# Optimization experiments

Measured on AMD Instinct MI355X. Metric: run time of the kernel, lower is better.

## Reference

```python
import jax, jax.numpy as jnp
import numpy as np

NUM_HEADS = 16

def setup_inputs() -> dict:
    key = jax.random.key(0)
    ks = jax.random.split(key, 6)
    B, N, E = 2, 2048, 2048
    QK, V, M = 2048, 2048, 4096
    x = jax.random.normal(ks[0], (B, N, E), dtype=jnp.float32)
    Wq = jax.random.normal(ks[1], (QK, E), dtype=jnp.float32) * 0.02
    k_weight = jax.random.normal(ks[2], (M, QK), dtype=jnp.float32) * 0.05
    v_weight = jax.random.normal(ks[3], (M, V), dtype=jnp.float32) * 0.05
    Wg = jax.random.normal(ks[4], (V, E), dtype=jnp.float32) * 0.02
    Wout = jax.random.normal(ks[5], (E, V), dtype=jnp.float32) * 0.02
    return {"x": x, "Wq": Wq, "k_weight": k_weight, "v_weight": v_weight, "Wg": Wg, "Wout": Wout}

def reference(x, Wq, k_weight, v_weight, Wg, Wout):
    H = NUM_HEADS
    B, N, E = x.shape
    M = k_weight.shape[0]
    # q: [B, N, QK] -> [B, H, N, dk]
    q = jnp.einsum('bne,fe->bnf', x, Wq)
    dk = q.shape[-1] // H
    q = q.reshape(B, N, H, dk).transpose(0, 2, 1, 3)
    # k: [M, QK] -> [H, M, dk]; v: [M, V] -> [H, M, dv]
    k = k_weight.reshape(M, H, dk).transpose(1, 0, 2)
    dv = v_weight.shape[1] // H
    v = v_weight.reshape(M, H, dv).transpose(1, 0, 2)
    scale = jnp.asarray(dk, x.dtype) ** 0.5  # use_scale == 1
    k = k * scale
    v = v * scale
    # non-softmax attention over fixed memory
    energy = jax.nn.silu(jnp.einsum('bhnd,hmd->bhnm', q, k))  # [B,H,N,M]
    out = jnp.einsum('bhnm,hmd->bhnd', energy, v)  # [B,H,N,dv]
    out = out.transpose(0, 2, 1, 3).reshape(B, N, H * dv)
    # output gate (silu)
    gate = jax.nn.silu(jnp.einsum('bne,ve->bnv', x, Wg))
    out = out * gate
    return jnp.einsum('bnv,ev->bne', out, Wout)
```

## Files before the change

kernel.cpp:

```cpp
#include <hip/hip_runtime.h>

typedef __bf16 bf16;
typedef __bf16 bf16x4 __attribute__((ext_vector_type(4)));
typedef __bf16 bf16x8 __attribute__((ext_vector_type(8)));
typedef float f32x4 __attribute__((ext_vector_type(4)));

#define MFMA(a, b, c) __builtin_amdgcn_mfma_f32_16x16x32_bf16(a, b, c, 0, 0, 0)

__device__ __forceinline__ float fast_silu(float x) {
  float e = __builtin_amdgcn_exp2f(x * -1.4426950408889634f);
  return x * __builtin_amdgcn_rcpf(1.f + e);
}

__device__ __forceinline__ void gload_lds16(const void* g, void* l) {
  __builtin_amdgcn_global_load_lds(
      (const __attribute__((address_space(1))) void*)g,
      (__attribute__((address_space(3))) void*)l, 16, 0, 0);
}

__global__ __launch_bounds__(256) void cvt_bf16(const float* __restrict__ in,
                                                bf16* __restrict__ out, int n) {
  int i = (blockIdx.x * 256 + threadIdx.x) * 4;
  if (i >= n) return;
  float4 v = *(const float4*)(in + i);
  bf16x4 o = {(bf16)v.x, (bf16)v.y, (bf16)v.z, (bf16)v.w};
  *(bf16x4*)(out + i) = o;
}

__global__ __launch_bounds__(256) void transpose_v_cvt(const float* __restrict__ v,
                                                       bf16* __restrict__ vt) {
  __shared__ bf16 T[64 * 72];
  const int m0 = blockIdx.x * 64, c0 = blockIdx.y * 64;
  const int tid = threadIdx.x;
  const int tr = tid >> 3;
  const int tc = (tid & 7) << 3;
#pragma unroll
  for (int it = 0; it < 2; it++) {
    int r = tr + it * 32;
    const float* src = v + (long)(m0 + r) * 2048 + c0 + tc;
    float4 a = *(const float4*)src;
    float4 b = *(const float4*)(src + 4);
    bf16x8 t = {(bf16)a.x, (bf16)a.y, (bf16)a.z, (bf16)a.w,
                (bf16)b.x, (bf16)b.y, (bf16)b.z, (bf16)b.w};
    *(bf16x8*)&T[r * 72 + tc] = t;
  }
  __syncthreads();
#pragma unroll
  for (int it = 0; it < 2; it++) {
    int c = tr + it * 32;
    bf16x8 o;
#pragma unroll
    for (int j = 0; j < 8; j++) o[j] = T[(tc + j) * 72 + c];
    *(bf16x8*)(vt + (long)(c0 + c) * 4096 + m0 + tc) = o;
  }
}

template <int MODE, int BM>
__global__ __launch_bounds__(512, 2) void gemm256(const bf16* __restrict__ A,
                                                  const bf16* __restrict__ B,
                                                  const bf16* __restrict__ B2,
                                                  bf16* __restrict__ C1,
                                                  bf16* __restrict__ C2,
                                                  float* __restrict__ Cf, int K, int N) {
  constexpr int MR = BM / 32;
  constexpr int MR2 = MR / 2;
  constexpr int NA = BM / 64;
  __shared__ bf16 As[2][BM * 64];
  __shared__ bf16 Bs[2][256 * 64];

  const int tid = threadIdx.x, wave = tid >> 6, lane = tid & 63;
  const int wr = wave >> 2, wc = wave & 3;
  const int quad = lane >> 4, fr = lane & 15;

  const int id2 = (blockIdx.x & 7) * 32 + (blockIdx.x >> 3);
  const int gx = (MODE == 3) ? (id2 >> 4) : (id2 >> 5);
  const int gy = (MODE == 3) ? (id2 & 15) : (id2 & 31);
  const bool gsel = (MODE == 3) && (gx >= 8);
  const bf16* Bm = gsel ? B2 : B;
  const long bM = (long)gy * BM;
  const long bN = (long)((MODE == 3) ? (gx & 7) : gx) * 256;

  f32x4 acc[MR][4] = {};

  const int srow = tid >> 3;
  const int sblk = (tid & 7) ^ (srow & 7);
  const bf16* Ag = A + (bM + srow) * (long)K + (sblk << 3);
  const bf16* Bg = Bm + (bN + srow) * (long)K + (sblk << 3);
  const int sdst = srow * 64 + ((tid & 7) << 3);

  auto stA = [&](int kt, int sb, int i) {
    gload_lds16(Ag + (long)i * 64 * K + kt * 64, &As[sb][sdst + i * 64 * 64]);
  };
  auto stB = [&](int kt, int sb, int i) {
    gload_lds16(Bg + (long)i * 64 * K + kt * 64, &Bs[sb][sdst + i * 64 * 64]);
  };
  auto rdA = [&](int rb, int mi, int kk) {
    int row = wr * (BM / 2) + mi * 16 + fr;
    return *(const bf16x8*)&As[rb][row * 64 + (((kk * 4 + quad) ^ (fr & 7)) << 3)];
  };
  auto rdB = [&](int rb, int ni, int kk) {
    int row = wc * 64 + ni * 16 + fr;
    return *(const bf16x8*)&Bs[rb][row * 64 + (((kk * 4 + quad) ^ (fr & 7)) << 3)];
  };

#pragma unroll
  for (int i = 0; i < NA; i++) stA(0, 0, i);
#pragma unroll
  for (int i = 0; i < 4; i++) stB(0, 0, i);
  __syncthreads();

  const int NT = K >> 6;
  for (int kt = 0; kt < NT; ++kt) {
    const int rb = kt & 1, sb = rb ^ 1;
    const bool st = (kt + 1) < NT;
    bf16x8 bfv[4][2], ah[MR2][2];

#pragma unroll
    for (int ni = 0; ni < 4; ni++)
#pragma unroll
      for (int kk = 0; kk < 2; kk++) bfv[ni][kk] = rdB(rb, ni, kk);
#pragma unroll
    for (int mi = 0; mi < MR2; mi++)
#pragma unroll
      for (int kk = 0; kk < 2; kk++) ah[mi][kk] = rdA(rb, mi, kk);
    if (st) {
      if (BM == 256) { stA(kt + 1, sb, 0); stA(kt + 1, sb, 1); }
      else { stA(kt + 1, sb, 0); stB(kt + 1, sb, 0); }
    }
    __builtin_amdgcn_s_barrier();
    __builtin_amdgcn_s_setprio(1);
#pragma unroll
    for (int mi = 0; mi < MR2; mi++)
#pragma unroll
      for (int ni = 0; ni < 2; ni++)
#pragma unroll
        for (int kk = 0; kk < 2; kk++) acc[mi][ni] = MFMA(ah[mi][kk], bfv[ni][kk], acc[mi][ni]);
    __builtin_amdgcn_s_setprio(0);
    __builtin_amdgcn_s_barrier();

    if (st) {
      if (BM == 256) { stA(kt + 1, sb, 2); stA(kt + 1, sb, 3); }
      else { stA(kt + 1, sb, 1); stB(kt + 1, sb, 1); }
    }
    __builtin_amdgcn_s_barrier();
    __builtin_amdgcn_s_setprio(1);
#pragma unroll
    for (int mi = 0; mi < MR2; mi++)
#pragma unroll
      for (int ni = 2; ni < 4; ni++)
#pragma unroll
        for (int kk = 0; kk < 2; kk++) acc[mi][ni] = MFMA(ah[mi][kk], bfv[ni][kk], acc[mi][ni]);
    __builtin_amdgcn_s_setprio(0);
    __builtin_amdgcn_s_barrier();

#pragma unroll
    for (int mi = 0; mi < MR2; mi++)
#pragma unroll
      for (int kk = 0; kk < 2; kk++) ah[mi][kk] = rdA(rb, mi + MR2, kk);
    if (st) {
      if (BM == 256) { stB(kt + 1, sb, 0); stB(kt + 1, sb, 1); }
      else { stB(kt + 1, sb, 2); }
    }
    __builtin_amdgcn_s_barrier();
    __builtin_amdgcn_s_setprio(1);
#pragma unroll
    for (int mi = 0; mi < MR2; mi++)
#pragma unroll
      for (int ni = 0; ni < 2; ni++)
#pragma unroll
        for (int kk = 0; kk < 2; kk++)
          acc[mi + MR2][ni] = MFMA(ah[mi][kk], bfv[ni][kk], acc[mi + MR2][ni]);
    __builtin_amdgcn_s_setprio(0);
    __builtin_amdgcn_s_barrier();

    if (st) {
      if (BM == 256) { stB(kt + 1, sb, 2); stB(kt + 1, sb, 3); }
      else { stB(kt + 1, sb, 3); }
    }
    __builtin_amdgcn_s_barrier();
    __builtin_amdgcn_s_setprio(1);
#pragma unroll
    for (int mi = 0; mi < MR2; mi++)
#pragma unroll
      for (int ni = 2; ni < 4; ni++)
#pragma unroll
        for (int kk = 0; kk < 2; kk++)
          acc[mi + MR2][ni] = MFMA(ah[mi][kk], bfv[ni][kk], acc[mi + MR2][ni]);
    __builtin_amdgcn_s_setprio(0);
    __syncthreads();
  }

#pragma unroll
  for (int mi = 0; mi < MR; mi++)
#pragma unroll
    for (int ni = 0; ni < 4; ni++)
#pragma unroll
      for (int r = 0; r < 4; r++) {
        long row = bM + wr * (BM / 2) + mi * 16 + quad * 4 + r;
        long col = bN + wc * 64 + ni * 16 + fr;
        float v = acc[mi][ni][r];
        if (MODE == 2) {
          Cf[row * (long)N + col] = v;
        } else {
          if (gsel)
            C2[row * (long)N + col] = (bf16)fast_silu(v);
          else
            C1[row * (long)N + col] = (bf16)(v * 11.3137085f);
        }
      }
}

__global__ __launch_bounds__(512, 4) void attn_fused(const bf16* __restrict__ q,
                                                     const bf16* __restrict__ kw,
                                                     const bf16* __restrict__ vt,
                                                     bf16* __restrict__ gate_io) {
  constexpr int E = 2048, M = 4096;
  constexpr float scale = 11.3137085f;
  const int bid = blockIdx.x;
  const int h = ((bid & 7) << 1) | ((bid >> 8) & 1);
  const int sub = (bid >> 3) & 31;
  const int b = sub >> 4, nt = sub & 15;
  const long n0 = (long)b * 2048 + nt * 128;

  const int tid = threadIdx.x, wave = tid >> 6, lane = tid & 63;
  const int quad = lane >> 4, ln = lane & 15;
  const int sw_m = wave & 1, sw_n = wave >> 1;
  const int pw_n = wave & 3, pw_dv = wave >> 2;

  __shared__ bf16 Ks[2][64 * 128];
  __shared__ bf16 Vts[2][128 * 64];
  __shared__ bf16 Ps[128 * 64];

  const bf16* qbase = q + (n0 + sw_n * 32) * E + h * 128;
  bf16x8 qf[2][4];
#pragma unroll
  for (int n2 = 0; n2 < 2; n2++)
#pragma unroll
    for (int ks = 0; ks < 4; ks++)
      qf[n2][ks] = *(const bf16x8*)(qbase + (long)(n2 * 16 + ln) * E + ks * 32 + (quad << 3));

  f32x4 oacc[2][4] = {};

  const bf16* kg = kw + (long)((wave << 3) + quad) * E + h * 128;
  const int ksl_off = (wave << 3) * 128 + lane * 8;
  int kc[2];
#pragma unroll
  for (int i = 0; i < 2; i++) kc[i] = (ln ^ ((wave * 8 + i * 4 + quad) & 15)) << 3;

  const bf16* vg = vt + (long)(h * 128 + (wave << 4) + (lane >> 3)) * M +
                   (((lane & 7) ^ ((lane >> 3) & 7)) << 3);
  const int vsl_off = (wave << 4) * 64 + lane * 8;

  int waddr[2][2];
#pragma unroll
  for (int mt = 0; mt < 2; mt++)
#pragma unroll
    for (int n2 = 0; n2 < 2; n2++) {
      int n = sw_n * 32 + n2 * 16 + ln;
      int mb8 = sw_m * 4 + mt * 2 + (quad >> 1);
      waddr[mt][n2] = n * 64 + ((mb8 ^ (n & 7)) << 3) + ((quad & 1) << 2);
    }

  auto stage = [&](int ms, int sb) {
#pragma unroll
    for (int i = 0; i < 2; i++) {
      gload_lds16(kg + (long)(ms + i * 4) * E + kc[i], &Ks[sb][ksl_off + i * 4 * 128]);
      gload_lds16(vg + ms + (long)i * 8 * M, &Vts[sb][vsl_off + i * 8 * 64]);
    }
  };

  stage(0, 0);
  asm volatile("s_waitcnt vmcnt(0)" ::: "memory");
  __builtin_amdgcn_s_barrier();

  auto body = [&](int m0, int rb, int sb, bool doStage) {
    if (doStage) stage(m0 + 64, sb);

    f32x4 sacc[2][2] = {};
    __builtin_amdgcn_s_setprio(1);
#pragma unroll
    for (int ks = 0; ks < 4; ks++) {
      bf16x8 af[2];
#pragma unroll
      for (int mt = 0; mt < 2; mt++)
        af[mt] = *(const bf16x8*)&Ks[rb][(sw_m * 32 + mt * 16 + ln) * 128 +
                                         (((ks * 4 + quad) ^ ln) << 3)];
#pragma unroll
      for (int mt = 0; mt < 2; mt++)
#pragma unroll
        for (int n2 = 0; n2 < 2; n2++) sacc[mt][n2] = MFMA(af[mt], qf[n2][ks], sacc[mt][n2]);
    }
    __builtin_amdgcn_s_setprio(0);

#pragma unroll
    for (int mt = 0; mt < 2; mt++)
#pragma unroll
      for (int n2 = 0; n2 < 2; n2++) {
        bf16x4 p;
#pragma unroll
        for (int r = 0; r < 4; r++) p[r] = (bf16)fast_silu(sacc[mt][n2][r]);
        *(bf16x4*)&Ps[waddr[mt][n2]] = p;
      }

    asm volatile("s_waitcnt lgkmcnt(0)" ::: "memory");
    __builtin_amdgcn_s_barrier();

#pragma unroll
    for (int ks = 0; ks < 2; ks++) {
      const int so = ((ks * 4 + quad) ^ (ln & 7)) << 3;
      bf16x8 pf[2], vf[4];
#pragma unroll
      for (int n2 = 0; n2 < 2; n2++)
        pf[n2] = *(const bf16x8*)&Ps[(pw_n * 32 + n2 * 16 + ln) * 64 + so];
#pragma unroll
      for (int dt = 0; dt < 4; dt++)
        vf[dt] = *(const bf16x8*)&Vts[rb][(pw_dv * 64 + dt * 16 + ln) * 64 + so];
      __builtin_amdgcn_s_setprio(1);
#pragma unroll
      for (int n2 = 0; n2 < 2; n2++)
#pragma unroll
        for (int dt = 0; dt < 4; dt++) oacc[n2][dt] = MFMA(pf[n2], vf[dt], oacc[n2][dt]);
      __builtin_amdgcn_s_setprio(0);
    }

    asm volatile("s_waitcnt vmcnt(0)" ::: "memory");
    __builtin_amdgcn_s_barrier();
  };

  for (int m0 = 0; m0 < M; m0 += 128) {
    body(m0, 0, 1, true);
    body(m0 + 64, 1, 0, m0 + 128 < M);
  }

  bf16* gio = gate_io + n0 * E + h * 128;
#pragma unroll
  for (int n2 = 0; n2 < 2; n2++)
#pragma unroll
    for (int dt = 0; dt < 4; dt++)
#pragma unroll
      for (int r = 0; r < 4; r++) {
        int n = pw_n * 32 + n2 * 16 + quad * 4 + r;
        int dv = pw_dv * 64 + dt * 16 + ln;
        float g = (float)gio[(long)n * E + dv];
        gio[(long)n * E + dv] = (bf16)(g * oacc[n2][dt][r] * scale);
      }
}

extern "C" void kernel_launch(void* const* d_in, const int* in_sizes, int n_in,
                              void* d_out, int out_size, void* d_ws, size_t ws_size,
                              hipStream_t stream) {
  const float* x = (const float*)d_in[0];
  const float* Wq = (const float*)d_in[1];
  const float* kw = (const float*)d_in[2];
  const float* vw = (const float*)d_in[3];
  const float* Wg = (const float*)d_in[4];
  const float* Wout = (const float*)d_in[5];
  float* out = (float*)d_out;
  bf16* ws = (bf16*)d_ws;

  bf16* S0 = ws;
  bf16* S1 = ws + 8388608;
  bf16* S2 = ws + 16777216;
  bf16* S3 = ws + 25165824;
  bf16* S4 = ws + 33554432;
  bf16* Wgb = S1 + 4194304;

  cvt_bf16<<<8192, 256, 0, stream>>>(x, S0, 8388608);
  cvt_bf16<<<4096, 256, 0, stream>>>(Wq, S1, 4194304);
  cvt_bf16<<<4096, 256, 0, stream>>>(Wg, Wgb, 4194304);
  transpose_v_cvt<<<dim3(64, 32), 256, 0, stream>>>(vw, S2);
  gemm256<3, 256><<<256, 512, 0, stream>>>(S0, S1, Wgb, S3, S4, (float*)nullptr, 2048, 2048);
  cvt_bf16<<<8192, 256, 0, stream>>>(kw, S0, 8388608);
  attn_fused<<<512, 512, 0, stream>>>(S3, S0, S2, S4);
  cvt_bf16<<<4096, 256, 0, stream>>>(Wout, S1, 4194304);
  gemm256<2, 128><<<256, 512, 0, stream>>>(S4, S1, (const bf16*)nullptr, (bf16*)nullptr,
                                           (bf16*)nullptr, out, 2048, 2048);
}
```

Before: 460.3 us.

## Triple-buffer A tiles and issue all prefetches at iteration start with vmcnt waits

The GEMM main loop now triple-buffers the A tile and double-buffers B in LDS. All global-to-LDS loads for the next B tile and the A tile two steps ahead are issued at the top of each iteration, instead of being spread across four phases with extra barriers. The full __syncthreads is replaced by a partial s_waitcnt vmcnt plus s_barrier, so the A prefetch for kt+2 stays in flight across iterations and two barriers per iteration go away. In exchange, LDS use rises (the BM=256 variant needs about 160KB) and the tail iterations issue redundant loads of clamped tiles.

```diff
diff --git a/kernel.cpp b/kernel.cpp
--- a/kernel.cpp
+++ b/kernel.cpp
@@ -64,8 +64,8 @@
                                                   float* __restrict__ Cf, int K, int N) {
   constexpr int MR = BM / 32;
   constexpr int MR2 = MR / 2;
-  constexpr int NA = BM / 64;
-  __shared__ bf16 As[2][BM * 64];
+  constexpr int AL = BM / 64;
+  __shared__ bf16 As[3][BM * 64];
   __shared__ bf16 Bs[2][256 * 64];
 
   const int tid = threadIdx.x, wave = tid >> 6, lane = tid & 63;
@@ -88,33 +88,41 @@
   const bf16* Bg = Bm + (bN + srow) * (long)K + (sblk << 3);
   const int sdst = srow * 64 + ((tid & 7) << 3);
 
-  auto stA = [&](int kt, int sb, int i) {
-    gload_lds16(Ag + (long)i * 64 * K + kt * 64, &As[sb][sdst + i * 64 * 64]);
-  };
-  auto stB = [&](int kt, int sb, int i) {
-    gload_lds16(Bg + (long)i * 64 * K + kt * 64, &Bs[sb][sdst + i * 64 * 64]);
-  };
-  auto rdA = [&](int rb, int mi, int kk) {
+  auto stA = [&](int kt, int sb) {
+#pragma unroll
+    for (int i = 0; i < AL; i++)
+      gload_lds16(Ag + (long)i * 64 * K + kt * 64, &As[sb][sdst + i * 64 * 64]);
+  };
+  auto stB = [&](int kt, int sb) {
+#pragma unroll
+    for (int i = 0; i < 4; i++)
+      gload_lds16(Bg + (long)i * 64 * K + kt * 64, &Bs[sb][sdst + i * 64 * 64]);
+  };
+  auto rdA = [&](int ab, int mi, int kk) {
     int row = wr * (BM / 2) + mi * 16 + fr;
-    return *(const bf16x8*)&As[rb][row * 64 + (((kk * 4 + quad) ^ (fr & 7)) << 3)];
-  };
-  auto rdB = [&](int rb, int ni, int kk) {
+    return *(const bf16x8*)&As[ab][row * 64 + (((kk * 4 + quad) ^ (fr & 7)) << 3)];
+  };
+  auto rdB = [&](int bb, int ni, int kk) {
     int row = wc * 64 + ni * 16 + fr;
-    return *(const bf16x8*)&Bs[rb][row * 64 + (((kk * 4 + quad) ^ (fr & 7)) << 3)];
-  };
-
-#pragma unroll
-  for (int i = 0; i < NA; i++) stA(0, 0, i);
-#pragma unroll
-  for (int i = 0; i < 4; i++) stB(0, 0, i);
-  __syncthreads();
+    return *(const bf16x8*)&Bs[bb][row * 64 + (((kk * 4 + quad) ^ (fr & 7)) << 3)];
+  };
 
   const int NT = K >> 6;
+  stB(0, 0);
+  stA(0, 0);
+  stA(NT > 1 ? 1 : 0, 1);
+  if constexpr (AL == 4)
+    asm volatile("s_waitcnt vmcnt(4)" ::: "memory");
+  else
+    asm volatile("s_waitcnt vmcnt(2)" ::: "memory");
+  __builtin_amdgcn_s_barrier();
+
   for (int kt = 0; kt < NT; ++kt) {
-    const int rb = kt & 1, sb = rb ^ 1;
-    const bool st = (kt + 1) < NT;
+    const int ra = kt % 3, rb = kt & 1;
     bf16x8 bfv[4][2], ah[MR2][2];
 
+    stB(kt + 1 < NT ? kt + 1 : NT - 1, (kt + 1) & 1);
+    stA(kt + 2 < NT ? kt + 2 : NT - 1, (kt + 2) % 3);
 #pragma unroll
     for (int ni = 0; ni < 4; ni++)
 #pragma unroll
@@ -122,11 +130,7 @@
 #pragma unroll
     for (int mi = 0; mi < MR2; mi++)
 #pragma unroll
-      for (int kk = 0; kk < 2; kk++) ah[mi][kk] = rdA(rb, mi, kk);
-    if (st) {
-      if (BM == 256) { stA(kt + 1, sb, 0); stA(kt + 1, sb, 1); }
-      else { stA(kt + 1, sb, 0); stB(kt + 1, sb, 0); }
-    }
+      for (int kk = 0; kk < 2; kk++) ah[mi][kk] = rdA(ra, mi, kk);
     __builtin_amdgcn_s_barrier();
     __builtin_amdgcn_s_setprio(1);
 #pragma unroll
@@ -138,11 +142,6 @@
     __builtin_amdgcn_s_setprio(0);
     __builtin_amdgcn_s_barrier();
 
-    if (st) {
-      if (BM == 256) { stA(kt + 1, sb, 2); stA(kt + 1, sb, 3); }
-      else { stA(kt + 1, sb, 1); stB(kt + 1, sb, 1); }
-    }
-    __builtin_amdgcn_s_barrier();
     __builtin_amdgcn_s_setprio(1);
 #pragma unroll
     for (int mi = 0; mi < MR2; mi++)
@@ -156,11 +155,7 @@
 #pragma unroll
     for (int mi = 0; mi < MR2; mi++)
 #pragma unroll
-      for (int kk = 0; kk < 2; kk++) ah[mi][kk] = rdA(rb, mi + MR2, kk);
-    if (st) {
-      if (BM == 256) { stB(kt + 1, sb, 0); stB(kt + 1, sb, 1); }
-      else { stB(kt + 1, sb, 2); }
-    }
+      for (int kk = 0; kk < 2; kk++) ah[mi][kk] = rdA(ra, mi + MR2, kk);
     __builtin_amdgcn_s_barrier();
     __builtin_amdgcn_s_setprio(1);
 #pragma unroll
@@ -173,11 +168,6 @@
     __builtin_amdgcn_s_setprio(0);
     __builtin_amdgcn_s_barrier();
 
-    if (st) {
-      if (BM == 256) { stB(kt + 1, sb, 2); stB(kt + 1, sb, 3); }
-      else { stB(kt + 1, sb, 3); }
-    }
-    __builtin_amdgcn_s_barrier();
     __builtin_amdgcn_s_setprio(1);
 #pragma unroll
     for (int mi = 0; mi < MR2; mi++)
@@ -187,7 +177,11 @@
         for (int kk = 0; kk < 2; kk++)
           acc[mi + MR2][ni] = MFMA(ah[mi][kk], bfv[ni][kk], acc[mi + MR2][ni]);
     __builtin_amdgcn_s_setprio(0);
-    __syncthreads();
+    if constexpr (AL == 4)
+      asm volatile("s_waitcnt vmcnt(4)" ::: "memory");
+    else
+      asm volatile("s_waitcnt vmcnt(2)" ::: "memory");
+    __builtin_amdgcn_s_barrier();
   }
 
 #pragma unroll
```

After: 478.3 us. +3.9%, slower.

## Restructure attention kernel into smaller tiles with software-pipelined QK and PV stages

Applied to the files above, without the earlier changes.

The fused attention kernel now processes 64 query rows per block instead of 128, with 32-row memory chunks, and launches twice as many blocks at higher occupancy (launch bounds raised to 8). The loop is software-pipelined: the QK^T MFMA for chunk t overlaps with the PV MFMA for chunk t-1 through double-buffered P, K and V tiles, so only one barrier is needed per iteration. The aim is more latency hiding and better CU utilization. The cost is that each K/V tile is reused by fewer query rows, so total K/V traffic doubles, and there are more barriers per unit of work.

```diff
diff --git a/kernel.cpp b/kernel.cpp
--- a/kernel.cpp
+++ b/kernel.cpp
@@ -210,140 +210,108 @@
       }
 }
 
-__global__ __launch_bounds__(512, 4) void attn_fused(const bf16* __restrict__ q,
+__global__ __launch_bounds__(512, 8) void attn_fused(const bf16* __restrict__ q,
                                                      const bf16* __restrict__ kw,
                                                      const bf16* __restrict__ vt,
                                                      bf16* __restrict__ gate_io) {
-  constexpr int E = 2048, M = 4096;
+  constexpr int E = 2048, M = 4096, NT = 128;
   constexpr float scale = 11.3137085f;
   const int bid = blockIdx.x;
-  const int h = ((bid & 7) << 1) | ((bid >> 8) & 1);
-  const int sub = (bid >> 3) & 31;
-  const int b = sub >> 4, nt = sub & 15;
-  const long n0 = (long)b * 2048 + nt * 128;
+  const int h = ((bid & 7) << 1) | (bid >> 9);
+  const int sub = (bid >> 3) & 63;
+  const long n0 = (long)(sub >> 5) * 2048 + (sub & 31) * 64;
 
   const int tid = threadIdx.x, wave = tid >> 6, lane = tid & 63;
   const int quad = lane >> 4, ln = lane & 15;
   const int sw_m = wave & 1, sw_n = wave >> 1;
   const int pw_n = wave & 3, pw_dv = wave >> 2;
 
-  __shared__ bf16 Ks[2][64 * 128];
-  __shared__ bf16 Vts[2][128 * 64];
-  __shared__ bf16 Ps[128 * 64];
-
-  const bf16* qbase = q + (n0 + sw_n * 32) * E + h * 128;
-  bf16x8 qf[2][4];
-#pragma unroll
-  for (int n2 = 0; n2 < 2; n2++)
-#pragma unroll
-    for (int ks = 0; ks < 4; ks++)
-      qf[n2][ks] = *(const bf16x8*)(qbase + (long)(n2 * 16 + ln) * E + ks * 32 + (quad << 3));
-
-  f32x4 oacc[2][4] = {};
-
-  const bf16* kg = kw + (long)((wave << 3) + quad) * E + h * 128;
-  const int ksl_off = (wave << 3) * 128 + lane * 8;
-  int kc[2];
-#pragma unroll
-  for (int i = 0; i < 2; i++) kc[i] = (ln ^ ((wave * 8 + i * 4 + quad) & 15)) << 3;
-
-  const bf16* vg = vt + (long)(h * 128 + (wave << 4) + (lane >> 3)) * M +
-                   (((lane & 7) ^ ((lane >> 3) & 7)) << 3);
-  const int vsl_off = (wave << 4) * 64 + lane * 8;
-
-  int waddr[2][2];
-#pragma unroll
-  for (int mt = 0; mt < 2; mt++)
-#pragma unroll
-    for (int n2 = 0; n2 < 2; n2++) {
-      int n = sw_n * 32 + n2 * 16 + ln;
-      int mb8 = sw_m * 4 + mt * 2 + (quad >> 1);
-      waddr[mt][n2] = n * 64 + ((mb8 ^ (n & 7)) << 3) + ((quad & 1) << 2);
-    }
-
-  auto stage = [&](int ms, int sb) {
-#pragma unroll
-    for (int i = 0; i < 2; i++) {
-      gload_lds16(kg + (long)(ms + i * 4) * E + kc[i], &Ks[sb][ksl_off + i * 4 * 128]);
-      gload_lds16(vg + ms + (long)i * 8 * M, &Vts[sb][vsl_off + i * 8 * 64]);
-    }
-  };
-
-  stage(0, 0);
+  __shared__ bf16 Ks[2][32 * 128];
+  __shared__ bf16 Vts[2][128 * 32];
+  __shared__ bf16 Ps[2][64 * 32];
+
+  const bf16* qb = q + (n0 + sw_n * 16 + ln) * E + h * 128 + (quad << 3);
+  bf16x8 qf[4];
+#pragma unroll
+  for (int ks = 0; ks < 4; ks++) qf[ks] = *(const bf16x8*)(qb + ks * 32);
+
+  f32x4 oacc[4] = {};
+
+  const bf16* kg = kw + (long)(tid >> 4) * E + h * 128 +
+                   (((tid & 15) ^ ((tid >> 4) & 15)) << 3);
+  const bf16* vg = vt + (long)(h * 128 + (tid >> 2)) * M +
+                   (((tid & 3) ^ ((tid >> 3) & 3)) << 3);
+  const int ldst = tid * 8;
+
+  int aoff[4];
+#pragma unroll
+  for (int ks = 0; ks < 4; ks++)
+    aoff[ks] = (sw_m * 16 + ln) * 128 + (((ks * 4 + quad) ^ ln) << 3);
+  const int pwr = (sw_n * 16 + ln) * 32 + (((sw_m * 4 + quad) ^ (ln & 6)) << 2);
+  const int prd = (pw_n * 16 + ln) * 32 + ((quad ^ ((ln >> 1) & 3)) << 3);
+  int voff[4];
+#pragma unroll
+  for (int dt = 0; dt < 4; dt++)
+    voff[dt] = (pw_dv * 64 + dt * 16 + ln) * 32 + ((quad ^ ((ln >> 1) & 3)) << 3);
+
+  gload_lds16(kg, &Ks[0][ldst]);
   asm volatile("s_waitcnt vmcnt(0)" ::: "memory");
   __builtin_amdgcn_s_barrier();
 
-  auto body = [&](int m0, int rb, int sb, bool doStage) {
-    if (doStage) stage(m0 + 64, sb);
-
-    f32x4 sacc[2][2] = {};
+  for (int t = 0; t < NT; ++t) {
+    const int cur = t & 1, prv = cur ^ 1;
+    if (t + 1 < NT) gload_lds16(kg + (long)(t + 1) * 32 * E, &Ks[prv][ldst]);
+    gload_lds16(vg + t * 32, &Vts[cur][ldst]);
+
+    f32x4 sacc = {};
     __builtin_amdgcn_s_setprio(1);
 #pragma unroll
     for (int ks = 0; ks < 4; ks++) {
-      bf16x8 af[2];
-#pragma unroll
-      for (int mt = 0; mt < 2; mt++)
-        af[mt] = *(const bf16x8*)&Ks[rb][(sw_m * 32 + mt * 16 + ln) * 128 +
-                                         (((ks * 4 + quad) ^ ln) << 3)];
-#pragma unroll
-      for (int mt = 0; mt < 2; mt++)
-#pragma unroll
-        for (int n2 = 0; n2 < 2; n2++) sacc[mt][n2] = MFMA(af[mt], qf[n2][ks], sacc[mt][n2]);
-    }
-    __builtin_amdgcn_s_setprio(0);
-
-#pragma unroll
-    for (int mt = 0; mt < 2; mt++)
-#pragma unroll
-      for (int n2 = 0; n2 < 2; n2++) {
-        bf16x4 p;
-#pragma unroll
-        for (int r = 0; r < 4; r++) p[r] = (bf16)fast_silu(sacc[mt][n2][r]);
-        *(bf16x4*)&Ps[waddr[mt][n2]] = p;
+      bf16x8 af = *(const bf16x8*)&Ks[cur][aoff[ks]];
+      sacc = MFMA(af, qf[ks], sacc);
+    }
+    __builtin_amdgcn_s_setprio(0);
+
+    if (t > 0) {
+      bf16x8 pf = *(const bf16x8*)&Ps[prv][prd];
+      __builtin_amdgcn_s_setprio(1);
+#pragma unroll
+      for (int dt = 0; dt < 4; dt++) {
+        bf16x8 vf = *(const bf16x8*)&Vts[prv][voff[dt]];
+        oacc[dt] = MFMA(pf, vf, oacc[dt]);
       }
-
-    asm volatile("s_waitcnt lgkmcnt(0)" ::: "memory");
-    __builtin_amdgcn_s_barrier();
-
-#pragma unroll
-    for (int ks = 0; ks < 2; ks++) {
-      const int so = ((ks * 4 + quad) ^ (ln & 7)) << 3;
-      bf16x8 pf[2], vf[4];
-#pragma unroll
-      for (int n2 = 0; n2 < 2; n2++)
-        pf[n2] = *(const bf16x8*)&Ps[(pw_n * 32 + n2 * 16 + ln) * 64 + so];
-#pragma unroll
-      for (int dt = 0; dt < 4; dt++)
-        vf[dt] = *(const bf16x8*)&Vts[rb][(pw_dv * 64 + dt * 16 + ln) * 64 + so];
-      __builtin_amdgcn_s_setprio(1);
-#pragma unroll
-      for (int n2 = 0; n2 < 2; n2++)
-#pragma unroll
-        for (int dt = 0; dt < 4; dt++) oacc[n2][dt] = MFMA(pf[n2], vf[dt], oacc[n2][dt]);
       __builtin_amdgcn_s_setprio(0);
     }
 
-    asm volatile("s_waitcnt vmcnt(0)" ::: "memory");
-    __builtin_amdgcn_s_barrier();
-  };
-
-  for (int m0 = 0; m0 < M; m0 += 128) {
-    body(m0, 0, 1, true);
-    body(m0 + 64, 1, 0, m0 + 128 < M);
+    bf16x4 p;
+#pragma unroll
+    for (int r = 0; r < 4; r++) p[r] = (bf16)fast_silu(sacc[r]);
+    *(bf16x4*)&Ps[cur][pwr] = p;
+
+    asm volatile("s_waitcnt vmcnt(0) lgkmcnt(0)" ::: "memory");
+    __builtin_amdgcn_s_barrier();
+  }
+
+  {
+    constexpr int prv = (NT - 1) & 1;
+    bf16x8 pf = *(const bf16x8*)&Ps[prv][prd];
+#pragma unroll
+    for (int dt = 0; dt < 4; dt++) {
+      bf16x8 vf = *(const bf16x8*)&Vts[prv][voff[dt]];
+      oacc[dt] = MFMA(pf, vf, oacc[dt]);
+    }
   }
 
   bf16* gio = gate_io + n0 * E + h * 128;
 #pragma unroll
-  for (int n2 = 0; n2 < 2; n2++)
-#pragma unroll
-    for (int dt = 0; dt < 4; dt++)
-#pragma unroll
-      for (int r = 0; r < 4; r++) {
-        int n = pw_n * 32 + n2 * 16 + quad * 4 + r;
-        int dv = pw_dv * 64 + dt * 16 + ln;
-        float g = (float)gio[(long)n * E + dv];
-        gio[(long)n * E + dv] = (bf16)(g * oacc[n2][dt][r] * scale);
-      }
+  for (int dt = 0; dt < 4; dt++)
+#pragma unroll
+    for (int r = 0; r < 4; r++) {
+      int n = pw_n * 16 + quad * 4 + r;
+      int dv = pw_dv * 64 + dt * 16 + ln;
+      float g = (float)gio[(long)n * E + dv];
+      gio[(long)n * E + dv] = (bf16)(g * oacc[dt][r] * scale);
+    }
 }
 
 extern "C" void kernel_launch(void* const* d_in, const int* in_sizes, int n_in,
@@ -371,7 +339,7 @@
   transpose_v_cvt<<<dim3(64, 32), 256, 0, stream>>>(vw, S2);
   gemm256<3, 256><<<256, 512, 0, stream>>>(S0, S1, Wgb, S3, S4, (float*)nullptr, 2048, 2048);
   cvt_bf16<<<8192, 256, 0, stream>>>(kw, S0, 8388608);
-  attn_fused<<<512, 512, 0, stream>>>(S3, S0, S2, S4);
+  attn_fused<<<1024, 512, 0, stream>>>(S3, S0, S2, S4);
   cvt_bf16<<<4096, 256, 0, stream>>>(Wout, S1, 4194304);
   gemm256<2, 128><<<256, 512, 0, stream>>>(S4, S1, (const bf16*)nullptr, (bf16*)nullptr,
                                            (bf16*)nullptr, out, 2048, 2048);
```

After: 498.9 us. 1.08x slower.
